# Kernel tuning notes

Measured on AMD Instinct MI355X. Metric: run time of the kernel, lower is better.

Reference implementation:

```python
import jax, jax.numpy as jnp
import numpy as np

N_NODES = 50000


def gcn_conv(x, W, b, src, dst):
    # PyG GCNConv: lin (no bias) -> add self-loops -> symmetric deg norm ->
    # scatter-add messages to target nodes -> add bias.
    n = x.shape[0]
    xw = x @ W  # [N, H]
    loops = jnp.arange(n, dtype=src.dtype)
    s = jnp.concatenate([src, loops])
    d = jnp.concatenate([dst, loops])
    deg = jax.ops.segment_sum(jnp.ones(d.shape[0], dtype=x.dtype), d, num_segments=n)
    dinv = deg ** -0.5  # deg >= 1 due to self-loops
    norm = dinv[s] * dinv[d]  # [E+N]
    msg = xw[s] * norm[:, None]  # gather + scale, [E+N, H]
    out = jax.ops.segment_sum(msg, d, num_segments=n)  # scatter-add
    return out + b


def setup_inputs() -> dict:
    key = jax.random.key(0)
    ks = jax.random.split(key, 8)
    in_feats, hidden, out_feats, p = 64, 64, 32, 4
    x = jax.random.normal(ks[0], (N_NODES, in_feats), dtype=jnp.float32)
    edge_index = jax.random.randint(ks[1], (2, 800000), 0, N_NODES, dtype=jnp.int64)
    s1 = (1.0 / in_feats) ** 0.5
    s2 = (1.0 / hidden) ** 0.5
    W1 = jax.random.uniform(ks[2], (in_feats, hidden), jnp.float32, -s1, s1)
    b1 = jnp.zeros((hidden,), jnp.float32)
    W2 = jax.random.uniform(ks[3], (hidden, hidden), jnp.float32, -s2, s2)
    b2 = jnp.zeros((hidden,), jnp.float32)
    Wr = jax.random.uniform(ks[4], (hidden, out_feats * p), jnp.float32, -s2, s2)
    br = jax.random.uniform(ks[5], (out_feats * p,), jnp.float32, -s2, s2)
    return {"x": x, "edge_index": edge_index, "W1": W1, "b1": b1,
            "W2": W2, "b2": b2, "Wr": Wr, "br": br}


def reference(x, edge_index, W1, b1, W2, b2, Wr, br):
    src, dst = edge_index[0], edge_index[1]
    h = jax.nn.relu(gcn_conv(x, W1, b1, src, dst))
    h = jax.nn.relu(gcn_conv(h, W2, b2, src, dst))
    g = jnp.mean(h, axis=0, keepdims=True)  # [1, hidden]
    out = (g @ Wr + br).reshape(32, 4)  # (out_feats, p)
    return out
```

## Files before the change

### kernel.cpp

```cpp
#include <hip/hip_runtime.h>
#include <math.h>


#define CH 4096
#define MAXNB 1024
#define SCL 2097152.0f
#define INVSCL 4.76837158203125e-7f

__device__ __forceinline__ float bf2f(unsigned short u) {
    return __uint_as_float(((unsigned)u) << 16);
}
__device__ __forceinline__ unsigned short f2bf(float x) {
    unsigned b = __float_as_uint(x);
    return (unsigned short)((b + 0x7FFF + ((b >> 16) & 1)) >> 16);
}

__global__ __launch_bounds__(256) void k_bucket_hist(const int* __restrict__ dst,
                                                     int* __restrict__ histmat,
                                                     int E, int NB) {
    __shared__ int ih[MAXNB];
    int t = threadIdx.x;
    for (int k = t; k < NB; k += 256) ih[k] = 0;
    __syncthreads();
    int base = blockIdx.x * CH;
    for (int i = 0; i < CH; i += 256) {
        int e = base + i + t;
        if (e < E) atomicAdd(&ih[dst[e] >> 6], 1);
    }
    __syncthreads();
    for (int k = t; k < NB; k += 256) histmat[(size_t)blockIdx.x * NB + k] = ih[k];
}

__global__ __launch_bounds__(1024) void k_scan(int* __restrict__ histmat,
                                               int* __restrict__ bstart,
                                               float* __restrict__ gpart,
                                               int NB, int nch, int E) {
    __shared__ int sc[1024];
    int t = threadIdx.x;
    int run = 0;
    if (t < NB) {
        int b = 0;
        for (; b + 8 <= nch; b += 8) {
            int v[8];
#pragma unroll
            for (int u = 0; u < 8; u++) v[u] = histmat[(size_t)(b + u) * NB + t];
#pragma unroll
            for (int u = 0; u < 8; u++) {
                int x = v[u];
                histmat[(size_t)(b + u) * NB + t] = run;
                run += x;
            }
        }
        for (; b < nch; b++) {
            int x = histmat[(size_t)b * NB + t];
            histmat[(size_t)b * NB + t] = run;
            run += x;
        }
    }
    sc[t] = (t < NB) ? run : 0;
    __syncthreads();
    for (int off = 1; off < 1024; off <<= 1) {
        int x = (t >= off) ? sc[t - off] : 0;
        __syncthreads();
        sc[t] += x;
        __syncthreads();
    }
    if (t < NB) bstart[t] = sc[t] - run;
    if (t == 0) bstart[NB] = E;
    if (t < 512) gpart[t] = 0.f;
}

__global__ __launch_bounds__(256) void k_bucket_scatter(const int* __restrict__ src,
                                                        const int* __restrict__ dst,
                                                        const int* __restrict__ histmat,
                                                        const int* __restrict__ bstart,
                                                        int* __restrict__ staged,
                                                        int E, int NB) {
    __shared__ int cur[MAXNB];
    int t = threadIdx.x;
    for (int k = t; k < NB; k += 256)
        cur[k] = bstart[k] + histmat[(size_t)blockIdx.x * NB + k];
    __syncthreads();
    int base = blockIdx.x * CH;
    for (int i = 0; i < CH; i += 256) {
        int e = base + i + t;
        if (e < E) {
            int d = dst[e];
            int pos = atomicAdd(&cur[d >> 6], 1);
            staged[pos] = (src[e] << 6) | (d & 63);
        }
    }
}

__global__ __launch_bounds__(256) void k_dinv_gemm(const float* __restrict__ X,
                                                   const float* __restrict__ W1,
                                                   const int* __restrict__ staged,
                                                   const int* __restrict__ bstart,
                                                   float* __restrict__ dinv,
                                                   unsigned short* __restrict__ Y, int n) {
    __shared__ float Ws[64 * 64];
    __shared__ float xs[16][64];
    __shared__ int cnt[64];
    __shared__ float dvs[64];
    int t = threadIdx.x, w = t >> 6, f = t & 63;
    int kb = blockIdx.x;
    if (t < 64) cnt[t] = 0;
    {
        const float4* W4 = (const float4*)W1;
        float4* Ws4 = (float4*)Ws;
#pragma unroll
        for (int j = 0; j < 4; j++) Ws4[t + 256 * j] = W4[t + 256 * j];
    }
    __syncthreads();
    int beg = bstart[kb], end = bstart[kb + 1];
    for (int e = beg + t; e < end; e += 256) atomicAdd(&cnt[staged[e] & 63], 1);
    __syncthreads();
    if (t < 64) {
        float dv = 1.0f / sqrtf((float)(cnt[t] + 1));
        dvs[t] = dv;
        int node = kb * 64 + t;
        if (node < n) dinv[node] = dv;
    }
    __syncthreads();
    for (int sub = 0; sub < 4; sub++) {
        int rb = kb * 64 + sub * 16;
#pragma unroll
        for (int i = 0; i < 4; i++) {
            int r = rb + w * 4 + i;
            xs[w * 4 + i][f] = (r < n) ? X[(size_t)r * 64 + f] : 0.f;
        }
        __syncthreads();
        float acc0 = 0.f, acc1 = 0.f, acc2 = 0.f, acc3 = 0.f;
#pragma unroll
        for (int kq = 0; kq < 16; kq++) {
            float wv0 = Ws[(4 * kq + 0) * 64 + f];
            float wv1 = Ws[(4 * kq + 1) * 64 + f];
            float wv2 = Ws[(4 * kq + 2) * 64 + f];
            float wv3 = Ws[(4 * kq + 3) * 64 + f];
            float4 x0 = *(const float4*)&xs[w * 4 + 0][4 * kq];
            float4 x1 = *(const float4*)&xs[w * 4 + 1][4 * kq];
            float4 x2 = *(const float4*)&xs[w * 4 + 2][4 * kq];
            float4 x3 = *(const float4*)&xs[w * 4 + 3][4 * kq];
            acc0 += x0.x * wv0 + x0.y * wv1 + x0.z * wv2 + x0.w * wv3;
            acc1 += x1.x * wv0 + x1.y * wv1 + x1.z * wv2 + x1.w * wv3;
            acc2 += x2.x * wv0 + x2.y * wv1 + x2.z * wv2 + x2.w * wv3;
            acc3 += x3.x * wv0 + x3.y * wv1 + x3.z * wv2 + x3.w * wv3;
        }
        float av[4] = {acc0, acc1, acc2, acc3};
#pragma unroll
        for (int i = 0; i < 4; i++) {
            int r = rb + w * 4 + i;
            if (r < n) Y[(size_t)r * 64 + f] = f2bf(dvs[sub * 16 + w * 4 + i] * av[i]);
        }
        __syncthreads();
    }
}

__global__ __launch_bounds__(256) void k_agg1(const unsigned short* __restrict__ Yin,
                                              const float* __restrict__ dinv,
                                              const float* __restrict__ b1,
                                              const int* __restrict__ staged,
                                              const int* __restrict__ bstart,
                                              const float* __restrict__ W2,
                                              unsigned short* __restrict__ Yout, int n) {
    __shared__ int accL[64 * 68];
    __shared__ float Ws[64 * 64];
    __shared__ float dvs[64];
    float* accF = (float*)accL;
    int t = threadIdx.x, w = t >> 6, l = t & 63;
    int kb = blockIdx.x;
    {
        int4* a4 = (int4*)accL;
        int4 z = make_int4(0, 0, 0, 0);
        for (int i = t; i < 64 * 17; i += 256) a4[i] = z;
        int m = t >> 2, seg = t & 3;
        int fm = ((m & 15) << 2) | (m >> 4);
        const float4* W24 = (const float4*)W2;
        float4* Ws4 = (float4*)Ws;
#pragma unroll
        for (int k = 0; k < 4; k++) Ws4[m * 16 + seg * 4 + k] = W24[fm * 16 + seg * 4 + k];
        if (t < 64) {
            int node = kb * 64 + t;
            dvs[t] = (node < n) ? dinv[node] : 0.f;
        }
    }
    __syncthreads();
    int beg = bstart[kb], end = bstart[kb + 1];
    int c = l & 15;
    int S = t >> 4;
    const ushort4* Y4 = (const ushort4*)Yin;
    int eb = beg + S * 4;
    int pk[4];
#pragma unroll
    for (int u = 0; u < 4; u++) pk[u] = (eb + u < end) ? staged[eb + u] : -1;
    for (; eb < end;) {
        int en = eb + 64;
        int pn[4];
#pragma unroll
        for (int u = 0; u < 4; u++) pn[u] = (en + u < end) ? staged[en + u] : -1;
#pragma unroll
        for (int u = 0; u < 4; u++) {
            int p = pk[u];
            if (p >= 0) {
                int s = p >> 6, dl = p & 63;
                ushort4 v = Y4[(size_t)s * 16 + c];
                int* ap = &accL[dl * 68 + c];
                atomicAdd(ap + 0,  __float2int_rn(bf2f(v.x) * SCL));
                atomicAdd(ap + 16, __float2int_rn(bf2f(v.y) * SCL));
                atomicAdd(ap + 32, __float2int_rn(bf2f(v.z) * SCL));
                atomicAdd(ap + 48, __float2int_rn(bf2f(v.w) * SCL));
            }
        }
#pragma unroll
        for (int u = 0; u < 4; u++) pk[u] = pn[u];
        eb = en;
    }
    __syncthreads();
    {
        int r = t >> 2, qd = t & 3;
        int node = kb * 64 + r;
        float dv = dvs[r];
        bool valid = node < n;
#pragma unroll
        for (int jj = 0; jj < 16; jj++) {
            int m = qd * 16 + jj;
            int fm = (jj << 2) | qd;
            float aggv = (float)accL[r * 68 + m] * INVSCL;
            float self = valid ? bf2f(Yin[(size_t)node * 64 + fm]) : 0.f;
            float hv = fmaxf(dv * (aggv + self) + b1[fm], 0.f);
            accF[r * 68 + m] = dv * hv;
        }
        if (!valid) {
#pragma unroll
            for (int jj = 0; jj < 16; jj++) accF[r * 68 + qd * 16 + jj] = 0.f;
        }
    }
    __syncthreads();
    float acc2[16];
#pragma unroll
    for (int r = 0; r < 16; r++) acc2[r] = 0.f;
    for (int q = 0; q < 16; q++) {
        float wv0 = Ws[(4 * q + 0) * 64 + l];
        float wv1 = Ws[(4 * q + 1) * 64 + l];
        float wv2 = Ws[(4 * q + 2) * 64 + l];
        float wv3 = Ws[(4 * q + 3) * 64 + l];
#pragma unroll
        for (int r = 0; r < 16; r++) {
            float4 h4 = *(const float4*)&accF[(w * 16 + r) * 68 + 4 * q];
            acc2[r] += h4.x * wv0 + h4.y * wv1 + h4.z * wv2 + h4.w * wv3;
        }
    }
#pragma unroll
    for (int r = 0; r < 16; r++) {
        int node = kb * 64 + w * 16 + r;
        if (node < n) Yout[(size_t)node * 64 + l] = f2bf(acc2[r]);
    }
}

__global__ __launch_bounds__(256) void k_agg2(const unsigned short* __restrict__ Yin,
                                              const float* __restrict__ dinv,
                                              const float* __restrict__ b2,
                                              const int* __restrict__ staged,
                                              const int* __restrict__ bstart,
                                              float* __restrict__ gpart, int n) {
    __shared__ int accL[64 * 68];
    __shared__ float dvs[64];
    __shared__ float part[4][64];
    int t = threadIdx.x, w = t >> 6, l = t & 63;
    int kb = blockIdx.x;
    {
        int4* a4 = (int4*)accL;
        int4 z = make_int4(0, 0, 0, 0);
        for (int i = t; i < 64 * 17; i += 256) a4[i] = z;
        if (t < 64) {
            int node = kb * 64 + t;
            dvs[t] = (node < n) ? dinv[node] : 0.f;
        }
    }
    __syncthreads();
    int beg = bstart[kb], end = bstart[kb + 1];
    int c = l & 15;
    int S = t >> 4;
    const ushort4* Y4 = (const ushort4*)Yin;
    int eb = beg + S * 4;
    int pk[4];
#pragma unroll
    for (int u = 0; u < 4; u++) pk[u] = (eb + u < end) ? staged[eb + u] : -1;
    for (; eb < end;) {
        int en = eb + 64;
        int pn[4];
#pragma unroll
        for (int u = 0; u < 4; u++) pn[u] = (en + u < end) ? staged[en + u] : -1;
#pragma unroll
        for (int u = 0; u < 4; u++) {
            int p = pk[u];
            if (p >= 0) {
                int s = p >> 6, dl = p & 63;
                ushort4 v = Y4[(size_t)s * 16 + c];
                int* ap = &accL[dl * 68 + c];
                atomicAdd(ap + 0,  __float2int_rn(bf2f(v.x) * SCL));
                atomicAdd(ap + 16, __float2int_rn(bf2f(v.y) * SCL));
                atomicAdd(ap + 32, __float2int_rn(bf2f(v.z) * SCL));
                atomicAdd(ap + 48, __float2int_rn(bf2f(v.w) * SCL));
            }
        }
#pragma unroll
        for (int u = 0; u < 4; u++) pk[u] = pn[u];
        eb = en;
    }
    __syncthreads();
    int m = l;
    int fm = ((m & 15) << 2) | (m >> 4);
    float bb = b2[fm];
    float local = 0.f;
#pragma unroll
    for (int i = 0; i < 16; i++) {
        int r = w * 16 + i;
        int node = kb * 64 + r;
        if (node < n) {
            float dv = dvs[r];
            float aggv = (float)accL[r * 68 + m] * INVSCL;
            float self = bf2f(Yin[(size_t)node * 64 + fm]);
            local += fmaxf(dv * (aggv + self) + bb, 0.f);
        }
    }
    part[w][m] = local;
    __syncthreads();
    if (t < 64) {
        float tot = part[0][t] + part[1][t] + part[2][t] + part[3][t];
        int fm2 = ((t & 15) << 2) | (t >> 4);
        atomicAdd(&gpart[((kb & 7) << 6) + fm2], tot);
    }
}

__global__ void k_readout(const float* __restrict__ gpart, const float* __restrict__ Wr,
                          const float* __restrict__ br, float* __restrict__ out,
                          float invn) {
    __shared__ float gl[64];
    int t = threadIdx.x;
    if (t < 64) {
        float s = 0.f;
#pragma unroll
        for (int j = 0; j < 8; j++) s += gpart[j * 64 + t];
        gl[t] = s * invn;
    }
    __syncthreads();
    float acc = br[t];
#pragma unroll
    for (int k = 0; k < 64; k++) acc += gl[k] * Wr[k * 128 + t];
    out[t] = acc;
}

extern "C" void kernel_launch(void* const* d_in, const int* in_sizes, int n_in,
                              void* d_out, int out_size, void* d_ws, size_t ws_size,
                              hipStream_t stream) {
    const float* x  = (const float*)d_in[0];
    const int*   ei = (const int*)d_in[1];
    const float* W1 = (const float*)d_in[2];
    const float* b1 = (const float*)d_in[3];
    const float* W2 = (const float*)d_in[4];
    const float* b2 = (const float*)d_in[5];
    const float* Wr = (const float*)d_in[6];
    const float* br = (const float*)d_in[7];
    float* out = (float*)d_out;

    int n = in_sizes[0] / 64;
    int E = in_sizes[1] / 2;
    const int* src = ei;
    const int* dst = ei + E;

    int NB  = (n + 63) / 64;
    int nch = (E + CH - 1) / CH;

    char* p = (char*)d_ws;
    unsigned short* y1 = (unsigned short*)p; p += (size_t)n * 64 * sizeof(unsigned short);
    unsigned short* y2 = (unsigned short*)p; p += (size_t)n * 64 * sizeof(unsigned short);
    float* dinv = (float*)p;   p += (size_t)n * sizeof(float);
    float* gpart = (float*)p;  p += 512 * sizeof(float);
    int* staged = (int*)p;     p += (size_t)E * sizeof(int);
    int* histmat = (int*)p;    p += (size_t)nch * NB * sizeof(int);
    int* bstart = (int*)p;     p += (size_t)(NB + 1) * sizeof(int);

    k_bucket_hist<<<nch, 256, 0, stream>>>(dst, histmat, E, NB);
    k_scan<<<1, 1024, 0, stream>>>(histmat, bstart, gpart, NB, nch, E);
    k_bucket_scatter<<<nch, 256, 0, stream>>>(src, dst, histmat, bstart, staged, E, NB);
    k_dinv_gemm<<<NB, 256, 0, stream>>>(x, W1, staged, bstart, dinv, y1, n);
    k_agg1<<<NB, 256, 0, stream>>>(y1, dinv, b1, staged, bstart, W2, y2, n);
    k_agg2<<<NB, 256, 0, stream>>>(y2, dinv, b2, staged, bstart, gpart, n);
    k_readout<<<1, 128, 0, stream>>>(gpart, Wr, br, out, 1.0f / (float)n);
}
```

Baseline: 259.9 us.

## Split dinv from layer-1 GEMM and widen aggregation blocks to 512 threads

The fused degree-count plus GEMM kernel becomes two kernels: a small per-bucket degree kernel and a GEMM kernel with 16 rows per block, which gives many more blocks. The two aggregation kernels now run 512 threads per block, so twice as many edges are processed at once per 64-node bucket, and the epilogue work is re-split across 8 waves. The aim is more parallelism and better latency hiding in the gather and atomic phase. The cost is an extra kernel launch, and the GEMM kernel reloads W into shared memory for every 16-row block.

Measured after the change: 451.8 us. +73.8%, slower.

```diff
diff --git a/kernel.cpp b/kernel.cpp
--- a/kernel.cpp
+++ b/kernel.cpp
@@ -92,71 +92,55 @@
     }
 }
 
-__global__ __launch_bounds__(256) void k_dinv_gemm(const float* __restrict__ X,
-                                                   const float* __restrict__ W1,
-                                                   const int* __restrict__ staged,
-                                                   const int* __restrict__ bstart,
-                                                   float* __restrict__ dinv,
-                                                   unsigned short* __restrict__ Y, int n) {
+__global__ __launch_bounds__(256) void k_dinv(const int* __restrict__ staged,
+                                              const int* __restrict__ bstart,
+                                              float* __restrict__ dinv, int n) {
+    __shared__ int cnt[64];
+    int t = threadIdx.x, kb = blockIdx.x;
+    if (t < 64) cnt[t] = 0;
+    __syncthreads();
+    int beg = bstart[kb], end = bstart[kb + 1];
+    for (int e = beg + t; e < end; e += 256) atomicAdd(&cnt[staged[e] & 63], 1);
+    __syncthreads();
+    if (t < 64) {
+        int node = kb * 64 + t;
+        if (node < n) dinv[node] = 1.0f / sqrtf((float)(cnt[t] + 1));
+    }
+}
+
+__global__ __launch_bounds__(256) void k_gemm_scale(const float* __restrict__ X,
+                                                    const float* __restrict__ W,
+                                                    const float* __restrict__ dinv,
+                                                    unsigned short* __restrict__ Y, int n) {
     __shared__ float Ws[64 * 64];
     __shared__ float xs[16][64];
-    __shared__ int cnt[64];
-    __shared__ float dvs[64];
     int t = threadIdx.x, w = t >> 6, f = t & 63;
-    int kb = blockIdx.x;
-    if (t < 64) cnt[t] = 0;
-    {
-        const float4* W4 = (const float4*)W1;
-        float4* Ws4 = (float4*)Ws;
-#pragma unroll
-        for (int j = 0; j < 4; j++) Ws4[t + 256 * j] = W4[t + 256 * j];
-    }
-    __syncthreads();
-    int beg = bstart[kb], end = bstart[kb + 1];
-    for (int e = beg + t; e < end; e += 256) atomicAdd(&cnt[staged[e] & 63], 1);
-    __syncthreads();
-    if (t < 64) {
-        float dv = 1.0f / sqrtf((float)(cnt[t] + 1));
-        dvs[t] = dv;
-        int node = kb * 64 + t;
-        if (node < n) dinv[node] = dv;
-    }
-    __syncthreads();
-    for (int sub = 0; sub < 4; sub++) {
-        int rb = kb * 64 + sub * 16;
-#pragma unroll
-        for (int i = 0; i < 4; i++) {
-            int r = rb + w * 4 + i;
-            xs[w * 4 + i][f] = (r < n) ? X[(size_t)r * 64 + f] : 0.f;
-        }
-        __syncthreads();
-        float acc0 = 0.f, acc1 = 0.f, acc2 = 0.f, acc3 = 0.f;
-#pragma unroll
-        for (int kq = 0; kq < 16; kq++) {
-            float wv0 = Ws[(4 * kq + 0) * 64 + f];
-            float wv1 = Ws[(4 * kq + 1) * 64 + f];
-            float wv2 = Ws[(4 * kq + 2) * 64 + f];
-            float wv3 = Ws[(4 * kq + 3) * 64 + f];
-            float4 x0 = *(const float4*)&xs[w * 4 + 0][4 * kq];
-            float4 x1 = *(const float4*)&xs[w * 4 + 1][4 * kq];
-            float4 x2 = *(const float4*)&xs[w * 4 + 2][4 * kq];
-            float4 x3 = *(const float4*)&xs[w * 4 + 3][4 * kq];
-            acc0 += x0.x * wv0 + x0.y * wv1 + x0.z * wv2 + x0.w * wv3;
-            acc1 += x1.x * wv0 + x1.y * wv1 + x1.z * wv2 + x1.w * wv3;
-            acc2 += x2.x * wv0 + x2.y * wv1 + x2.z * wv2 + x2.w * wv3;
-            acc3 += x3.x * wv0 + x3.y * wv1 + x3.z * wv2 + x3.w * wv3;
-        }
-        float av[4] = {acc0, acc1, acc2, acc3};
-#pragma unroll
-        for (int i = 0; i < 4; i++) {
-            int r = rb + w * 4 + i;
-            if (r < n) Y[(size_t)r * 64 + f] = f2bf(dvs[sub * 16 + w * 4 + i] * av[i]);
-        }
-        __syncthreads();
-    }
-}
-
-__global__ __launch_bounds__(256) void k_agg1(const unsigned short* __restrict__ Yin,
+    const float4* W4 = (const float4*)W;
+    float4* Ws4 = (float4*)Ws;
+#pragma unroll
+    for (int j = 0; j < 4; j++) Ws4[t + 256 * j] = W4[t + 256 * j];
+    int r0 = blockIdx.x * 16;
+#pragma unroll
+    for (int i = 0; i < 4; i++) {
+        int r = r0 + w * 4 + i;
+        xs[w * 4 + i][f] = (r < n) ? X[(size_t)r * 64 + f] : 0.f;
+    }
+    __syncthreads();
+    float acc[4] = {0.f, 0.f, 0.f, 0.f};
+#pragma unroll 8
+    for (int k = 0; k < 64; k++) {
+        float wv = Ws[k * 64 + f];
+#pragma unroll
+        for (int i = 0; i < 4; i++) acc[i] += xs[w * 4 + i][k] * wv;
+    }
+#pragma unroll
+    for (int i = 0; i < 4; i++) {
+        int r = r0 + w * 4 + i;
+        if (r < n) Y[(size_t)r * 64 + f] = f2bf(dinv[r] * acc[i]);
+    }
+}
+
+__global__ __launch_bounds__(512) void k_agg1(const unsigned short* __restrict__ Yin,
                                               const float* __restrict__ dinv,
                                               const float* __restrict__ b1,
                                               const int* __restrict__ staged,
@@ -172,13 +156,13 @@
     {
         int4* a4 = (int4*)accL;
         int4 z = make_int4(0, 0, 0, 0);
-        for (int i = t; i < 64 * 17; i += 256) a4[i] = z;
-        int m = t >> 2, seg = t & 3;
+        for (int i = t; i < 64 * 17; i += 512) a4[i] = z;
+        int m = t >> 3, seg = t & 7;
         int fm = ((m & 15) << 2) | (m >> 4);
         const float4* W24 = (const float4*)W2;
         float4* Ws4 = (float4*)Ws;
 #pragma unroll
-        for (int k = 0; k < 4; k++) Ws4[m * 16 + seg * 4 + k] = W24[fm * 16 + seg * 4 + k];
+        for (int k = 0; k < 2; k++) Ws4[m * 16 + seg * 2 + k] = W24[fm * 16 + seg * 2 + k];
         if (t < 64) {
             int node = kb * 64 + t;
             dvs[t] = (node < n) ? dinv[node] : 0.f;
@@ -186,7 +170,7 @@
     }
     __syncthreads();
     int beg = bstart[kb], end = bstart[kb + 1];
-    int c = l & 15;
+    int c = t & 15;
     int S = t >> 4;
     const ushort4* Y4 = (const ushort4*)Yin;
     int eb = beg + S * 4;
@@ -194,7 +178,7 @@
 #pragma unroll
     for (int u = 0; u < 4; u++) pk[u] = (eb + u < end) ? staged[eb + u] : -1;
     for (; eb < end;) {
-        int en = eb + 64;
+        int en = eb + 128;
         int pn[4];
 #pragma unroll
         for (int u = 0; u < 4; u++) pn[u] = (en + u < end) ? staged[en + u] : -1;
@@ -217,47 +201,43 @@
     }
     __syncthreads();
     {
-        int r = t >> 2, qd = t & 3;
+        int r = t >> 3, g8 = t & 7;
         int node = kb * 64 + r;
         float dv = dvs[r];
         bool valid = node < n;
 #pragma unroll
-        for (int jj = 0; jj < 16; jj++) {
-            int m = qd * 16 + jj;
-            int fm = (jj << 2) | qd;
+        for (int jj = 0; jj < 8; jj++) {
+            int m = g8 * 8 + jj;
+            int fm = ((m & 15) << 2) | (m >> 4);
             float aggv = (float)accL[r * 68 + m] * INVSCL;
             float self = valid ? bf2f(Yin[(size_t)node * 64 + fm]) : 0.f;
             float hv = fmaxf(dv * (aggv + self) + b1[fm], 0.f);
-            accF[r * 68 + m] = dv * hv;
-        }
-        if (!valid) {
-#pragma unroll
-            for (int jj = 0; jj < 16; jj++) accF[r * 68 + qd * 16 + jj] = 0.f;
-        }
-    }
-    __syncthreads();
-    float acc2[16];
-#pragma unroll
-    for (int r = 0; r < 16; r++) acc2[r] = 0.f;
+            accF[r * 68 + m] = valid ? dv * hv : 0.f;
+        }
+    }
+    __syncthreads();
+    float acc2[8];
+#pragma unroll
+    for (int r = 0; r < 8; r++) acc2[r] = 0.f;
     for (int q = 0; q < 16; q++) {
         float wv0 = Ws[(4 * q + 0) * 64 + l];
         float wv1 = Ws[(4 * q + 1) * 64 + l];
         float wv2 = Ws[(4 * q + 2) * 64 + l];
         float wv3 = Ws[(4 * q + 3) * 64 + l];
 #pragma unroll
-        for (int r = 0; r < 16; r++) {
-            float4 h4 = *(const float4*)&accF[(w * 16 + r) * 68 + 4 * q];
+        for (int r = 0; r < 8; r++) {
+            float4 h4 = *(const float4*)&accF[(w * 8 + r) * 68 + 4 * q];
             acc2[r] += h4.x * wv0 + h4.y * wv1 + h4.z * wv2 + h4.w * wv3;
         }
     }
 #pragma unroll
-    for (int r = 0; r < 16; r++) {
-        int node = kb * 64 + w * 16 + r;
+    for (int r = 0; r < 8; r++) {
+        int node = kb * 64 + w * 8 + r;
         if (node < n) Yout[(size_t)node * 64 + l] = f2bf(acc2[r]);
     }
 }
 
-__global__ __launch_bounds__(256) void k_agg2(const unsigned short* __restrict__ Yin,
+__global__ __launch_bounds__(512) void k_agg2(const unsigned short* __restrict__ Yin,
                                               const float* __restrict__ dinv,
                                               const float* __restrict__ b2,
                                               const int* __restrict__ staged,
@@ -265,13 +245,13 @@
                                               float* __restrict__ gpart, int n) {
     __shared__ int accL[64 * 68];
     __shared__ float dvs[64];
-    __shared__ float part[4][64];
+    __shared__ float part[8][64];
     int t = threadIdx.x, w = t >> 6, l = t & 63;
     int kb = blockIdx.x;
     {
         int4* a4 = (int4*)accL;
         int4 z = make_int4(0, 0, 0, 0);
-        for (int i = t; i < 64 * 17; i += 256) a4[i] = z;
+        for (int i = t; i < 64 * 17; i += 512) a4[i] = z;
         if (t < 64) {
             int node = kb * 64 + t;
             dvs[t] = (node < n) ? dinv[node] : 0.f;
@@ -279,7 +259,7 @@
     }
     __syncthreads();
     int beg = bstart[kb], end = bstart[kb + 1];
-    int c = l & 15;
+    int c = t & 15;
     int S = t >> 4;
     const ushort4* Y4 = (const ushort4*)Yin;
     int eb = beg + S * 4;
@@ -287,7 +267,7 @@
 #pragma unroll
     for (int u = 0; u < 4; u++) pk[u] = (eb + u < end) ? staged[eb + u] : -1;
     for (; eb < end;) {
-        int en = eb + 64;
+        int en = eb + 128;
         int pn[4];
 #pragma unroll
         for (int u = 0; u < 4; u++) pn[u] = (en + u < end) ? staged[en + u] : -1;
@@ -314,8 +294,8 @@
     float bb = b2[fm];
     float local = 0.f;
 #pragma unroll
-    for (int i = 0; i < 16; i++) {
-        int r = w * 16 + i;
+    for (int i = 0; i < 8; i++) {
+        int r = w * 8 + i;
         int node = kb * 64 + r;
         if (node < n) {
             float dv = dvs[r];
@@ -327,7 +307,9 @@
     part[w][m] = local;
     __syncthreads();
     if (t < 64) {
-        float tot = part[0][t] + part[1][t] + part[2][t] + part[3][t];
+        float tot = 0.f;
+#pragma unroll
+        for (int r = 0; r < 8; r++) tot += part[r][t];
         int fm2 = ((t & 15) << 2) | (t >> 4);
         atomicAdd(&gpart[((kb & 7) << 6) + fm2], tot);
     }
@@ -384,8 +366,9 @@
     k_bucket_hist<<<nch, 256, 0, stream>>>(dst, histmat, E, NB);
     k_scan<<<1, 1024, 0, stream>>>(histmat, bstart, gpart, NB, nch, E);
     k_bucket_scatter<<<nch, 256, 0, stream>>>(src, dst, histmat, bstart, staged, E, NB);
-    k_dinv_gemm<<<NB, 256, 0, stream>>>(x, W1, staged, bstart, dinv, y1, n);
-    k_agg1<<<NB, 256, 0, stream>>>(y1, dinv, b1, staged, bstart, W2, y2, n);
-    k_agg2<<<NB, 256, 0, stream>>>(y2, dinv, b2, staged, bstart, gpart, n);
+    k_dinv<<<NB, 256, 0, stream>>>(staged, bstart, dinv, n);
+    k_gemm_scale<<<(n + 15) / 16, 256, 0, stream>>>(x, W1, dinv, y1, n);
+    k_agg1<<<NB, 512, 0, stream>>>(y1, dinv, b1, staged, bstart, W2, y2, n);
+    k_agg2<<<NB, 512, 0, stream>>>(y2, dinv, b2, staged, bstart, gpart, n);
     k_readout<<<1, 128, 0, stream>>>(gpart, Wr, br, out, 1.0f / (float)n);
 }
```
